# Kernel optimization log

Hardware: AMD Instinct MI355X
Metric: run time of the kernel (lower is better)

Reference implementation:

```python
import jax, jax.numpy as jnp
import numpy as np
from jax import lax

KSIZE = 3
STRIDE = 1
RATE = 2
FUSE_K = 3
SCALE = 10.0
DN = ('NCHW', 'OIHW', 'NCHW')


def _same_pad_amount(size, k, s):
    out = (size + s - 1) // s
    pad = max(0, (out - 1) * s + k - size)
    return pad // 2, pad - pad // 2


def extract_patches(x, k, s):
    # torch.nn.Unfold with 'same' padding; returns [B, L, C, k, k], L row-major
    B, C, H, W = x.shape
    pt, pb = _same_pad_amount(H, k, s)
    pl, pr = _same_pad_amount(W, k, s)
    xp = jnp.pad(x, ((0, 0), (0, 0), (pt, pb), (pl, pr)))
    Ho = (H + s - 1) // s
    Wo = (W + s - 1) // s
    rows = (jnp.arange(Ho) * s)[:, None] + jnp.arange(k)[None, :]  # [Ho,k]
    cols = (jnp.arange(Wo) * s)[:, None] + jnp.arange(k)[None, :]  # [Wo,k]
    p = xp[:, :, rows, :][:, :, :, :, cols]  # [B,C,Ho,k,Wo,k]
    return p.transpose(0, 2, 4, 1, 3, 5).reshape(B, Ho * Wo, C, k, k)


def setup_inputs() -> dict:
    key = jax.random.key(0)
    kf, kb = jax.random.split(key)
    f = jax.random.normal(kf, (2, 128, 128, 128), dtype=jnp.float32)
    b = jax.random.normal(kb, (2, 128, 128, 128), dtype=jnp.float32)
    mask = jnp.zeros((1, 1, 128, 128), dtype=jnp.float32)  # all patches available
    return {"f": f, "b": b, "mask": mask}


def reference(f, b, mask):
    B, C, Hr, Wr = f.shape
    kernel = 2 * RATE
    # raw background patches for final aggregation: [B, Lb, C, 4, 4]
    raw_w = extract_patches(b, kernel, RATE * STRIDE)
    # nearest downsample by rate (src_idx = i*rate)
    f_ds = f[:, :, ::RATE, ::RATE]
    b_ds = b[:, :, ::RATE, ::RATE]
    Hf, Wf = f_ds.shape[2], f_ds.shape[3]
    Hb, Wb = b_ds.shape[2], b_ds.shape[3]
    L = Hb * Wb
    # matching patches: [B, L, C, 3, 3]
    w = extract_patches(b_ds, KSIZE, STRIDE)
    # mask patches (shared across batch, torch uses m[0])
    m_ds = mask[:, :, ::RATE, ::RATE]
    m = extract_patches(m_ds, KSIZE, STRIDE)[0]  # [L,1,3,3]
    mm = (jnp.mean(m, axis=(1, 2, 3)) == 0.0).astype(f.dtype).reshape(1, L, 1, 1)
    # L2-normalize patch filters (escape_NaN added elementwise before sum, as in torch)
    wn = w / jnp.sqrt(jnp.sum(w * w + 1e-4, axis=(2, 3, 4), keepdims=True))

    def score_one(xi, wi):
        # xi [C,Hf,Wf], wi [L,C,3,3] -> [L,Hf,Wf]
        return lax.conv_general_dilated(xi[None], wi, (1, 1), [(1, 1), (1, 1)],
                                        dimension_numbers=DN)[0]

    y = jax.vmap(score_one)(f_ds, wn)  # [B, L, Hf, Wf]

    # diagonal fuse: identity 3x3 conv on the [L, Hf*Wf] score matrix, twice with transpose
    fw = jnp.eye(FUSE_K, dtype=f.dtype).reshape(1, 1, FUSE_K, FUSE_K)

    def fuse_conv(t):
        return lax.conv_general_dilated(t, fw, (1, 1), [(1, 1), (1, 1)],
                                        dimension_numbers=DN)

    y = y.reshape(B, 1, Hb * Wb, Hf * Wf)
    y = fuse_conv(y).reshape(B, Hb, Wb, Hf, Wf)
    y = y.transpose(0, 2, 1, 4, 3).reshape(B, 1, L, Hf * Wf)
    y = fuse_conv(y).reshape(B, Wb, Hb, Wf, Hf)
    y = y.transpose(0, 2, 1, 4, 3).reshape(B, L, Hf, Wf)

    y = y * mm
    y = jax.nn.softmax(y * SCALE, axis=1) * mm

    def deconv_one(a, wc):
        # conv_transpose2d(a, wc, stride=rate, padding=1); wc [L,C,4,4]
        wt = jnp.flip(wc, (-2, -1)).transpose(1, 0, 2, 3)  # [C,L,4,4]
        pad = kernel - 1 - 1
        return lax.conv_general_dilated(a[None], wt, (1, 1), [(pad, pad), (pad, pad)],
                                        lhs_dilation=(RATE, RATE),
                                        dimension_numbers=DN)[0]

    out = jax.vmap(deconv_one)(y, raw_w) / 4.0  # [B, C, Hr, Wr]
    return out
```

## Files before the change

kernel.cpp:

```cpp
#include <hip/hip_runtime.h>
#include <cstdint>

typedef _Float16 f16x8 __attribute__((ext_vector_type(8)));
typedef float f32x4 __attribute__((ext_vector_type(4)));

typedef __attribute__((address_space(1))) void gvoid;
typedef __attribute__((address_space(3))) void lvoid;

__device__ __forceinline__ void gload16(const void* g, void* l) {
    __builtin_amdgcn_global_load_lds((gvoid*)g, (lvoid*)l, 16, 0, 0);
}

__device__ __forceinline__ void bar() {
    asm volatile("" ::: "memory");
    __builtin_amdgcn_s_barrier();
    asm volatile("" ::: "memory");
}
#define WAITV(N) asm volatile("s_waitcnt vmcnt(" #N ")" ::: "memory")

__global__ __launch_bounds__(256) void downsample_kernel(const float* __restrict__ f,
                                                         const float* __restrict__ b,
                                                         float* __restrict__ fds,
                                                         float* __restrict__ bds) {
    int idx = blockIdx.x * 256 + threadIdx.x;
    const float* src = blockIdx.y ? b : f;
    float* dst = blockIdx.y ? bds : fds;
    int bb = idx >> 19;
    int r = idx & 524287;
    int c = r >> 12, a = (r >> 6) & 63, v = r & 63;
    dst[idx] = src[(size_t)bb * 2097152 + (size_t)c * 16384 + (2 * a) * 128 + 2 * v];
}

__global__ __launch_bounds__(256) void build_mm_kernel(const float* __restrict__ mask,
                                                       float* __restrict__ mm) {
    int l = blockIdx.x * 256 + threadIdx.x;
    if (l >= 4096) return;
    int i = l >> 6, j = l & 63;
    float s = 0.f;
    #pragma unroll
    for (int dy = 0; dy < 3; ++dy)
        #pragma unroll
        for (int dx = 0; dx < 3; ++dx) {
            int a = i + dy - 1, b = j + dx - 1;
            if ((unsigned)a < 64u && (unsigned)b < 64u)
                s += mask[(2 * a) * 128 + 2 * b];
        }
    mm[l] = (s == 0.0f) ? 1.0f : 0.0f;
}

__global__ __launch_bounds__(256) void build_fpatch_kernel(const float* __restrict__ fds,
                                                           _Float16* __restrict__ Fp) {
    int bb = blockIdx.x >> 12;
    int p = blockIdx.x & 4095;
    const float* fb = fds + (size_t)bb * 524288;
    _Float16* Fpb = Fp + (size_t)bb * 4718592;
    int u = p >> 6, v = p & 63;
    for (int k = threadIdx.x; k < 1152; k += 256) {
        int c = k / 9;
        int s = k - 9 * c;
        int dy = s / 3, dx = s - 3 * dy;
        int a = u + dy - 1, bcol = v + dx - 1;
        float val = 0.f;
        if ((unsigned)a < 64u && (unsigned)bcol < 64u)
            val = fb[c * 4096 + a * 64 + bcol];
        Fpb[(size_t)p * 1152 + k] = (_Float16)val;
    }
}

__global__ __launch_bounds__(256) void build_wn_kernel(const float* __restrict__ bds,
                                                       _Float16* __restrict__ Wn) {
    __shared__ float wsh[1152];
    __shared__ float red[4];
    int bb = blockIdx.x >> 12;
    int l = blockIdx.x & 4095;
    const float* bp = bds + (size_t)bb * 524288;
    _Float16* Wnb = Wn + (size_t)bb * 4718592;
    int i = l >> 6, j = l & 63;
    float sq = 0.f;
    for (int k = threadIdx.x; k < 1152; k += 256) {
        int c = k / 9;
        int s = k - 9 * c;
        int dy = s / 3, dx = s - 3 * dy;
        int a = i + dy - 1, bcol = j + dx - 1;
        float val = 0.f;
        if ((unsigned)a < 64u && (unsigned)bcol < 64u)
            val = bp[c * 4096 + a * 64 + bcol];
        wsh[k] = val;
        sq += val * val;
    }
    #pragma unroll
    for (int off = 32; off > 0; off >>= 1) sq += __shfl_xor(sq, off);
    if ((threadIdx.x & 63) == 0) red[threadIdx.x >> 6] = sq;
    __syncthreads();
    float total = red[0] + red[1] + red[2] + red[3] + 0.1152f;
    float rinv = 1.0f / sqrtf(total);
    for (int k = threadIdx.x; k < 1152; k += 256)
        Wnb[(size_t)l * 1152 + k] = (_Float16)(wsh[k] * rinv);
}

__global__ __launch_bounds__(256) void build_vt_kernel(const float* __restrict__ b,
                                                       _Float16* __restrict__ Vt) {
    int bb = blockIdx.x >> 11;
    int n = blockIdx.x & 2047;
    const float* bp = b + (size_t)bb * 2097152;
    _Float16* Vtb = Vt + (size_t)bb * 8388608;
    int c = n >> 4, r = n & 15, rh = r >> 2, rw = r & 3;
    const float* bc = bp + (size_t)c * 16384;
    for (int l = threadIdx.x; l < 4096; l += 256) {
        int lh = l >> 6, lw = l & 63;
        int row = 2 * lh + rh - 1, col = 2 * lw + rw - 1;
        float val = 0.f;
        if ((unsigned)row < 128u && (unsigned)col < 128u)
            val = bc[row * 128 + col];
        Vtb[(size_t)n * 4096 + l] = (_Float16)val;
    }
}

__global__ __launch_bounds__(256) void gemm1_kernel(const _Float16* __restrict__ Fp,
                                                    const _Float16* __restrict__ Wn,
                                                    _Float16* __restrict__ S0) {
    __shared__ __align__(16) _Float16 As[128 * 32];
    __shared__ __align__(16) _Float16 Bs[128 * 32];
    const int z = blockIdx.z;
    const _Float16* A = Fp + (size_t)z * 4718592;
    const _Float16* Bt = Wn + (size_t)z * 4718592;
    _Float16* C = S0 + (size_t)z * 16777216;
    const int tid = threadIdx.x;
    const int lane = tid & 63;
    const int wave = tid >> 6;
    const int quad = lane >> 4;
    const int l16 = lane & 15;
    const int bm = blockIdx.y * 128;
    const int bn = blockIdx.x * 128;
    const int waveM = (wave >> 1) * 64;
    const int waveN = (wave & 1) * 64;
    const int K = 1152;

    f32x4 acc[4][4] = {};

    const int rowS = tid >> 2;
    const int colS = (tid & 3) * 8;

    for (int k0 = 0; k0 < K; k0 += 32) {
        #pragma unroll
        for (int i = 0; i < 2; ++i) {
            const _Float16* g = A + (size_t)(bm + i * 64 + rowS) * K + k0 + colS;
            gload16(g, &As[i * 2048 + tid * 8]);
        }
        #pragma unroll
        for (int i = 0; i < 2; ++i) {
            const _Float16* g = Bt + (size_t)(bn + i * 64 + rowS) * K + k0 + colS;
            gload16(g, &Bs[i * 2048 + tid * 8]);
        }
        __syncthreads();
        f16x8 a_frag[4], b_frag[4];
        #pragma unroll
        for (int mi = 0; mi < 4; ++mi)
            a_frag[mi] = *(const f16x8*)&As[(waveM + mi * 16 + l16) * 32 + quad * 8];
        #pragma unroll
        for (int ni = 0; ni < 4; ++ni)
            b_frag[ni] = *(const f16x8*)&Bs[(waveN + ni * 16 + l16) * 32 + quad * 8];
        #pragma unroll
        for (int mi = 0; mi < 4; ++mi)
            #pragma unroll
            for (int ni = 0; ni < 4; ++ni)
                acc[mi][ni] = __builtin_amdgcn_mfma_f32_16x16x32_f16(
                    a_frag[mi], b_frag[ni], acc[mi][ni], 0, 0, 0);
        __syncthreads();
    }

    #pragma unroll
    for (int mi = 0; mi < 4; ++mi)
        #pragma unroll
        for (int ni = 0; ni < 4; ++ni)
            #pragma unroll
            for (int r = 0; r < 4; ++r) {
                int row = bm + waveM + mi * 16 + quad * 4 + r;
                int col = bn + waveN + ni * 16 + l16;
                C[(size_t)row * 4096 + col] = (_Float16)acc[mi][ni][r];
            }
}

__global__ __launch_bounds__(512, 2) void gemm2_kernel(const _Float16* __restrict__ Vt,
                                                       const _Float16* __restrict__ att0,
                                                       const _Float16* __restrict__ att1,
                                                       _Float16* __restrict__ OTh) {
    __shared__ __align__(16) _Float16 As[2][2][8192];
    __shared__ __align__(16) _Float16 Bs[2][2][8192];
    const int z = blockIdx.z;
    const _Float16* A = Vt + (size_t)z * 8388608;
    const _Float16* Bt = z ? att1 : att0;
    _Float16* C = OTh + (size_t)z * 8388608;
    const int tid = threadIdx.x;
    const int lane = tid & 63;
    const int wave = tid >> 6;
    const int quad = lane >> 4;
    const int l16 = lane & 15;
    const int wm = wave >> 2;
    const int wn = wave & 3;
    const int bm = blockIdx.y * 256;
    const int bn = blockIdx.x * 256;

    f32x4 acc[8][4] = {};
    f16x8 afr[4], bfr[4];

    const int s0 = tid, s1 = 512 + tid;
    const int sr0 = s0 >> 2, sr1 = s1 >> 2;
    const int r0 = sr0 ^ ((sr0 >> 2) & 1);
    const int r1 = sr1 ^ ((sr1 >> 2) & 1);
    const int q0 = (s0 & 3) ^ (r0 & 3);
    const int q1 = (s1 & 3) ^ (r1 & 3);
    const int offA0 = (bm + r0) * 4096 + q0 * 8;
    const int offA1 = (bm + r1) * 4096 + q1 * 8;
    const int offB0 = (bn + r0) * 4096 + q0 * 8;
    const int offB1 = (bn + r1) * 4096 + q1 * 8;

#define STAGE_A(buf, kt, kh) do {                                          \
        gload16(A + offA0 + (kt) * 64 + (kh) * 32, &As[buf][kh][tid * 8]); \
        gload16(A + offA1 + (kt) * 64 + (kh) * 32, &As[buf][kh][4096 + tid * 8]); \
    } while (0)
#define STAGE_B(buf, kt, kh) do {                                          \
        gload16(Bt + offB0 + (kt) * 64 + (kh) * 32, &Bs[buf][kh][tid * 8]); \
        gload16(Bt + offB1 + (kt) * 64 + (kh) * 32, &Bs[buf][kh][4096 + tid * 8]); \
    } while (0)

    const int c2 = (l16 >> 2) & 1;
    const int rdoff = ((l16 ^ c2) * 32) + ((quad ^ (l16 & 3)) * 8);

    auto LDA = [&](int buf, int kh, int mh) {
        #pragma unroll
        for (int mi = 0; mi < 4; ++mi)
            afr[mi] = *(const f16x8*)&As[buf][kh][(wm * 128 + (mh * 4 + mi) * 16) * 32 + rdoff];
    };
    auto LDB = [&](int buf, int kh) {
        #pragma unroll
        for (int ni = 0; ni < 4; ++ni)
            bfr[ni] = *(const f16x8*)&Bs[buf][kh][(wn * 64 + ni * 16) * 32 + rdoff];
    };
    auto MM = [&](int mh) {
        __builtin_amdgcn_s_setprio(1);
        #pragma unroll
        for (int mi = 0; mi < 4; ++mi)
            #pragma unroll
            for (int ni = 0; ni < 4; ++ni)
                acc[mh * 4 + mi][ni] = __builtin_amdgcn_mfma_f32_16x16x32_f16(
                    afr[mi], bfr[ni], acc[mh * 4 + mi][ni], 0, 0, 0);
        __builtin_amdgcn_s_setprio(0);
    };

    STAGE_A(0, 0, 0); STAGE_B(0, 0, 0);
    STAGE_A(0, 0, 1); STAGE_B(0, 0, 1);
    STAGE_A(1, 1, 0); STAGE_B(1, 1, 0);
    WAITV(4);
    bar();

    #pragma unroll 1
    for (int i = 0; i < 31; ++i) {
        const int t0 = 2 * i;
        LDA(0, 0, 0); LDB(0, 0); STAGE_A(1, t0 + 1, 1);
        bar(); MM(0); bar();
        LDA(0, 0, 1); STAGE_B(1, t0 + 1, 1);
        bar(); MM(1); bar();
        LDA(0, 1, 0); LDB(0, 1); STAGE_A(0, t0 + 2, 0);
        bar(); MM(0); bar();
        LDA(0, 1, 1); STAGE_B(0, t0 + 2, 0);
        bar(); MM(1); WAITV(4); bar();
        LDA(1, 0, 0); LDB(1, 0); STAGE_A(0, t0 + 2, 1);
        bar(); MM(0); bar();
        LDA(1, 0, 1); STAGE_B(0, t0 + 2, 1);
        bar(); MM(1); bar();
        LDA(1, 1, 0); LDB(1, 1); STAGE_A(1, t0 + 3, 0);
        bar(); MM(0); bar();
        LDA(1, 1, 1); STAGE_B(1, t0 + 3, 0);
        bar(); MM(1); WAITV(4); bar();
    }

    LDA(0, 0, 0); LDB(0, 0); STAGE_A(1, 63, 1);
    bar(); MM(0); bar();
    LDA(0, 0, 1); STAGE_B(1, 63, 1);
    bar(); MM(1); bar();
    LDA(0, 1, 0); LDB(0, 1);
    bar(); MM(0); bar();
    LDA(0, 1, 1);
    bar(); MM(1); WAITV(0); bar();
    LDA(1, 0, 0); LDB(1, 0); bar(); MM(0); bar();
    LDA(1, 0, 1);            bar(); MM(1); bar();
    LDA(1, 1, 0); LDB(1, 1); bar(); MM(0); bar();
    LDA(1, 1, 1);            bar(); MM(1); bar();

#undef STAGE_A
#undef STAGE_B

    #pragma unroll
    for (int mi = 0; mi < 8; ++mi)
        #pragma unroll
        for (int ni = 0; ni < 4; ++ni)
            #pragma unroll
            for (int r = 0; r < 4; ++r) {
                int row = bm + wm * 128 + mi * 16 + quad * 4 + r;
                int col = bn + wn * 64 + ni * 16 + l16;
                C[(size_t)row * 4096 + col] = (_Float16)acc[mi][ni][r];
            }
}

__global__ __launch_bounds__(256) void fuse_softmax_kernel(const _Float16* __restrict__ S0,
                                                           const float* __restrict__ mm,
                                                           _Float16* __restrict__ att0,
                                                           _Float16* __restrict__ att1) {
    __shared__ float red[4];
    const int tid = threadIdx.x;
    const int lane = tid & 63;
    const int wave = tid >> 6;
    int g = blockIdx.x;
    int p_global = ((g & 7) << 10) | (g >> 3);
    const int bb = p_global >> 12;
    const int p = p_global & 4095;
    const _Float16* S = S0 + (size_t)bb * 16777216;
    _Float16* att = bb ? att1 : att0;
    const int pbase = ((p & 63) << 6) | (p >> 6);

    float acc[16];
    #pragma unroll
    for (int k = 0; k < 16; ++k) acc[k] = 0.f;

    #pragma unroll
    for (int t2 = -1; t2 <= 1; ++t2) {
        int b2 = pbase + t2;
        if ((unsigned)b2 >= 4096u) continue;
        int pp = ((b2 & 63) << 6) | (b2 >> 6);
        #pragma unroll
        for (int t1 = -1; t1 <= 1; ++t1) {
            int rr = pp + t1;
            if ((unsigned)rr >= 4096u) continue;
            const _Float16* row = S + (size_t)rr * 4096;
            #pragma unroll
            for (int k = 0; k < 16; ++k) {
                int l = k * 256 + tid;
                int i = (k * 256 + wave * 64) >> 6;
                int it2 = i + t2;
                if (it2 >= 0 && it2 < 64) {
                    int c = l + t2 * 64 + t1;
                    if ((unsigned)c < 4096u)
                        acc[k] += (float)row[c];
                } else if (it2 == 64) {
                    if (lane <= 62) {
                        int c = lane + 1 + t1;
                        if ((unsigned)c < 4096u) acc[k] += (float)row[c];
                    }
                } else {
                    if (lane >= 1) {
                        int c = 4031 + lane + t1;
                        if ((unsigned)c < 4096u) acc[k] += (float)row[c];
                    }
                }
            }
        }
    }

    float mv[16];
    float lmax = -1e30f;
    #pragma unroll
    for (int k = 0; k < 16; ++k) {
        int l = k * 256 + tid;
        mv[k] = mm[l];
        float lg = acc[k] * mv[k] * 10.0f;
        acc[k] = lg;
        lmax = fmaxf(lmax, lg);
    }
    #pragma unroll
    for (int off = 32; off > 0; off >>= 1) lmax = fmaxf(lmax, __shfl_xor(lmax, off));
    if (lane == 0) red[wave] = lmax;
    __syncthreads();
    lmax = fmaxf(fmaxf(red[0], red[1]), fmaxf(red[2], red[3]));
    __syncthreads();

    float lsum = 0.f;
    #pragma unroll
    for (int k = 0; k < 16; ++k) {
        float e = __expf(acc[k] - lmax);
        acc[k] = e;
        lsum += e;
    }
    #pragma unroll
    for (int off = 32; off > 0; off >>= 1) lsum += __shfl_xor(lsum, off);
    if (lane == 0) red[wave] = lsum;
    __syncthreads();
    float inv = 1.0f / (red[0] + red[1] + red[2] + red[3]);
    #pragma unroll
    for (int k = 0; k < 16; ++k) {
        int l = k * 256 + tid;
        att[(size_t)p * 4096 + l] = (_Float16)(acc[k] * inv * mv[k]);
    }
}

__global__ __launch_bounds__(256) void assemble_kernel(const _Float16* __restrict__ OTh,
                                                       float* __restrict__ out) {
    int idx = blockIdx.x * 256 + threadIdx.x;
    int bb = idx >> 21;
    int w = idx & 2097151;
    const _Float16* OTb = OTh + (size_t)bb * 8388608;
    int x = w & 127, y = (w >> 7) & 127, c = w >> 14;
    int r0 = (y + 1) & 1, s0 = (x + 1) & 1;
    float acc = 0.f;
    #pragma unroll
    for (int a = 0; a < 2; ++a) {
        int rh = r0 + 2 * a;
        int ph = (y + 1 - rh) >> 1;
        if ((unsigned)ph < 64u) {
            #pragma unroll
            for (int bq = 0; bq < 2; ++bq) {
                int rw = s0 + 2 * bq;
                int pw = (x + 1 - rw) >> 1;
                if ((unsigned)pw < 64u)
                    acc += (float)OTb[(size_t)(c * 16 + rh * 4 + rw) * 4096 + ph * 64 + pw];
            }
        }
    }
    out[idx] = 0.25f * acc;
}

extern "C" void kernel_launch(void* const* d_in, const int* in_sizes, int n_in,
                              void* d_out, int out_size, void* d_ws, size_t ws_size,
                              hipStream_t stream) {
    const float* f = (const float*)d_in[0];
    const float* b = (const float*)d_in[1];
    const float* mask = (const float*)d_in[2];
    float* out = (float*)d_out;
    char* ws = (char*)d_ws;

    float* mm = (float*)ws;
    _Float16* Fp = (_Float16*)(ws + 16384);
    _Float16* Wn = (_Float16*)(ws + 16384 + 18874368);
    _Float16* att0 = (_Float16*)(ws + 16384);
    _Float16* S0 = (_Float16*)(ws + 37765120);
    _Float16* Vt = (_Float16*)(ws + 37765120);
    _Float16* OTh = (_Float16*)(ws + 37765120 + 33554432);
    float* fds = (float*)(ws + 104873984);
    float* bds = (float*)(ws + 104873984 + 4194304);
    _Float16* att1 = (_Float16*)(ws + 104873984);

    downsample_kernel<<<dim3(4096, 2), 256, 0, stream>>>(f, b, fds, bds);
    build_mm_kernel<<<16, 256, 0, stream>>>(mask, mm);
    build_fpatch_kernel<<<8192, 256, 0, stream>>>(fds, Fp);
    build_wn_kernel<<<8192, 256, 0, stream>>>(bds, Wn);

    gemm1_kernel<<<dim3(32, 32, 2), 256, 0, stream>>>(Fp, Wn, S0);
    fuse_softmax_kernel<<<8192, 256, 0, stream>>>(S0, mm, att0, att1);

    build_vt_kernel<<<4096, 256, 0, stream>>>(b, Vt);
    gemm2_kernel<<<dim3(16, 8, 2), 512, 0, stream>>>(Vt, att0, att1, OTh);
    assemble_kernel<<<16384, 256, 0, stream>>>(OTh, out);
}
```

Measured before the change: 438.6 us.

## Rewrite score GEMM with 256x256 tiles, double-buffered LDS and swizzled layout

```diff
diff --git a/kernel.cpp b/kernel.cpp
--- a/kernel.cpp
+++ b/kernel.cpp
@@ -116,11 +116,11 @@
     }
 }
 
-__global__ __launch_bounds__(256) void gemm1_kernel(const _Float16* __restrict__ Fp,
-                                                    const _Float16* __restrict__ Wn,
-                                                    _Float16* __restrict__ S0) {
-    __shared__ __align__(16) _Float16 As[128 * 32];
-    __shared__ __align__(16) _Float16 Bs[128 * 32];
+__global__ __launch_bounds__(512, 2) void gemm1_kernel(const _Float16* __restrict__ Fp,
+                                                       const _Float16* __restrict__ Wn,
+                                                       _Float16* __restrict__ S0) {
+    __shared__ __align__(16) _Float16 As[2][2][8192];
+    __shared__ __align__(16) _Float16 Bs[2][2][8192];
     const int z = blockIdx.z;
     const _Float16* A = Fp + (size_t)z * 4718592;
     const _Float16* Bt = Wn + (size_t)z * 4718592;
@@ -130,53 +130,109 @@
     const int wave = tid >> 6;
     const int quad = lane >> 4;
     const int l16 = lane & 15;
-    const int bm = blockIdx.y * 128;
-    const int bn = blockIdx.x * 128;
-    const int waveM = (wave >> 1) * 64;
-    const int waveN = (wave & 1) * 64;
-    const int K = 1152;
-
-    f32x4 acc[4][4] = {};
-
-    const int rowS = tid >> 2;
-    const int colS = (tid & 3) * 8;
-
-    for (int k0 = 0; k0 < K; k0 += 32) {
-        #pragma unroll
-        for (int i = 0; i < 2; ++i) {
-            const _Float16* g = A + (size_t)(bm + i * 64 + rowS) * K + k0 + colS;
-            gload16(g, &As[i * 2048 + tid * 8]);
-        }
-        #pragma unroll
-        for (int i = 0; i < 2; ++i) {
-            const _Float16* g = Bt + (size_t)(bn + i * 64 + rowS) * K + k0 + colS;
-            gload16(g, &Bs[i * 2048 + tid * 8]);
-        }
-        __syncthreads();
-        f16x8 a_frag[4], b_frag[4];
+    const int wm = wave >> 2;
+    const int wn = wave & 3;
+    const int bm = blockIdx.y * 256;
+    const int bn = blockIdx.x * 256;
+
+    f32x4 acc[8][4] = {};
+    f16x8 afr[4], bfr[4];
+
+    const int s0 = tid, s1 = 512 + tid;
+    const int sr0 = s0 >> 2, sr1 = s1 >> 2;
+    const int r0 = sr0 ^ ((sr0 >> 2) & 1);
+    const int r1 = sr1 ^ ((sr1 >> 2) & 1);
+    const int q0 = (s0 & 3) ^ (r0 & 3);
+    const int q1 = (s1 & 3) ^ (r1 & 3);
+    const int offA0 = (bm + r0) * 1152 + q0 * 8;
+    const int offA1 = (bm + r1) * 1152 + q1 * 8;
+    const int offB0 = (bn + r0) * 1152 + q0 * 8;
+    const int offB1 = (bn + r1) * 1152 + q1 * 8;
+
+#define STAGE_A(buf, kt, kh) do {                                          \
+        gload16(A + offA0 + (kt) * 64 + (kh) * 32, &As[buf][kh][tid * 8]); \
+        gload16(A + offA1 + (kt) * 64 + (kh) * 32, &As[buf][kh][4096 + tid * 8]); \
+    } while (0)
+#define STAGE_B(buf, kt, kh) do {                                          \
+        gload16(Bt + offB0 + (kt) * 64 + (kh) * 32, &Bs[buf][kh][tid * 8]); \
+        gload16(Bt + offB1 + (kt) * 64 + (kh) * 32, &Bs[buf][kh][4096 + tid * 8]); \
+    } while (0)
+
+    const int c2 = (l16 >> 2) & 1;
+    const int rdoff = ((l16 ^ c2) * 32) + ((quad ^ (l16 & 3)) * 8);
+
+    auto LDA = [&](int buf, int kh, int mh) {
         #pragma unroll
         for (int mi = 0; mi < 4; ++mi)
-            a_frag[mi] = *(const f16x8*)&As[(waveM + mi * 16 + l16) * 32 + quad * 8];
+            afr[mi] = *(const f16x8*)&As[buf][kh][(wm * 128 + (mh * 4 + mi) * 16) * 32 + rdoff];
+    };
+    auto LDB = [&](int buf, int kh) {
         #pragma unroll
         for (int ni = 0; ni < 4; ++ni)
-            b_frag[ni] = *(const f16x8*)&Bs[(waveN + ni * 16 + l16) * 32 + quad * 8];
+            bfr[ni] = *(const f16x8*)&Bs[buf][kh][(wn * 64 + ni * 16) * 32 + rdoff];
+    };
+    auto MM = [&](int mh) {
+        __builtin_amdgcn_s_setprio(1);
         #pragma unroll
         for (int mi = 0; mi < 4; ++mi)
             #pragma unroll
             for (int ni = 0; ni < 4; ++ni)
-                acc[mi][ni] = __builtin_amdgcn_mfma_f32_16x16x32_f16(
-                    a_frag[mi], b_frag[ni], acc[mi][ni], 0, 0, 0);
-        __syncthreads();
-    }
-
-    #pragma unroll
-    for (int mi = 0; mi < 4; ++mi)
+                acc[mh * 4 + mi][ni] = __builtin_amdgcn_mfma_f32_16x16x32_f16(
+                    afr[mi], bfr[ni], acc[mh * 4 + mi][ni], 0, 0, 0);
+        __builtin_amdgcn_s_setprio(0);
+    };
+
+    STAGE_A(0, 0, 0); STAGE_B(0, 0, 0);
+    STAGE_A(0, 0, 1); STAGE_B(0, 0, 1);
+    STAGE_A(1, 1, 0); STAGE_B(1, 1, 0);
+    WAITV(4);
+    bar();
+
+    #pragma unroll 1
+    for (int i = 0; i < 8; ++i) {
+        const int t0 = 2 * i;
+        LDA(0, 0, 0); LDB(0, 0); STAGE_A(1, t0 + 1, 1);
+        bar(); MM(0); bar();
+        LDA(0, 0, 1); STAGE_B(1, t0 + 1, 1);
+        bar(); MM(1); bar();
+        LDA(0, 1, 0); LDB(0, 1); STAGE_A(0, t0 + 2, 0);
+        bar(); MM(0); bar();
+        LDA(0, 1, 1); STAGE_B(0, t0 + 2, 0);
+        bar(); MM(1); WAITV(4); bar();
+        LDA(1, 0, 0); LDB(1, 0); STAGE_A(0, t0 + 2, 1);
+        bar(); MM(0); bar();
+        LDA(1, 0, 1); STAGE_B(0, t0 + 2, 1);
+        bar(); MM(1); bar();
+        LDA(1, 1, 0); LDB(1, 1); STAGE_A(1, t0 + 3, 0);
+        bar(); MM(0); bar();
+        LDA(1, 1, 1); STAGE_B(1, t0 + 3, 0);
+        bar(); MM(1); WAITV(4); bar();
+    }
+
+    LDA(0, 0, 0); LDB(0, 0); STAGE_A(1, 17, 1);
+    bar(); MM(0); bar();
+    LDA(0, 0, 1); STAGE_B(1, 17, 1);
+    bar(); MM(1); bar();
+    LDA(0, 1, 0); LDB(0, 1);
+    bar(); MM(0); bar();
+    LDA(0, 1, 1);
+    bar(); MM(1); WAITV(0); bar();
+    LDA(1, 0, 0); LDB(1, 0); bar(); MM(0); bar();
+    LDA(1, 0, 1);            bar(); MM(1); bar();
+    LDA(1, 1, 0); LDB(1, 1); bar(); MM(0); bar();
+    LDA(1, 1, 1);            bar(); MM(1); bar();
+
+#undef STAGE_A
+#undef STAGE_B
+
+    #pragma unroll
+    for (int mi = 0; mi < 8; ++mi)
         #pragma unroll
         for (int ni = 0; ni < 4; ++ni)
             #pragma unroll
             for (int r = 0; r < 4; ++r) {
-                int row = bm + waveM + mi * 16 + quad * 4 + r;
-                int col = bn + waveN + ni * 16 + l16;
+                int row = bm + wm * 128 + mi * 16 + quad * 4 + r;
+                int col = bn + wn * 64 + ni * 16 + l16;
                 C[(size_t)row * 4096 + col] = (_Float16)acc[mi][ni][r];
             }
 }
@@ -444,7 +500,7 @@
     build_fpatch_kernel<<<8192, 256, 0, stream>>>(fds, Fp);
     build_wn_kernel<<<8192, 256, 0, stream>>>(bds, Wn);
 
-    gemm1_kernel<<<dim3(32, 32, 2), 256, 0, stream>>>(Fp, Wn, S0);
+    gemm1_kernel<<<dim3(16, 16, 2), 512, 0, stream>>>(Fp, Wn, S0);
     fuse_softmax_kernel<<<8192, 256, 0, stream>>>(S0, mm, att0, att1);
 
     build_vt_kernel<<<4096, 256, 0, stream>>>(b, Vt);
```

New measurement: 434.2 us. About the same (-1.0%).

## Share pipelined 256x256 GEMM core across both GEMMs with register double-buffered fragments

Applied to the files above, without the earlier changes.

```diff
diff --git a/kernel.cpp b/kernel.cpp
--- a/kernel.cpp
+++ b/kernel.cpp
@@ -116,81 +116,12 @@
     }
 }
 
-__global__ __launch_bounds__(256) void gemm1_kernel(const _Float16* __restrict__ Fp,
-                                                    const _Float16* __restrict__ Wn,
-                                                    _Float16* __restrict__ S0) {
-    __shared__ __align__(16) _Float16 As[128 * 32];
-    __shared__ __align__(16) _Float16 Bs[128 * 32];
-    const int z = blockIdx.z;
-    const _Float16* A = Fp + (size_t)z * 4718592;
-    const _Float16* Bt = Wn + (size_t)z * 4718592;
-    _Float16* C = S0 + (size_t)z * 16777216;
-    const int tid = threadIdx.x;
-    const int lane = tid & 63;
-    const int wave = tid >> 6;
-    const int quad = lane >> 4;
-    const int l16 = lane & 15;
-    const int bm = blockIdx.y * 128;
-    const int bn = blockIdx.x * 128;
-    const int waveM = (wave >> 1) * 64;
-    const int waveN = (wave & 1) * 64;
-    const int K = 1152;
-
-    f32x4 acc[4][4] = {};
-
-    const int rowS = tid >> 2;
-    const int colS = (tid & 3) * 8;
-
-    for (int k0 = 0; k0 < K; k0 += 32) {
-        #pragma unroll
-        for (int i = 0; i < 2; ++i) {
-            const _Float16* g = A + (size_t)(bm + i * 64 + rowS) * K + k0 + colS;
-            gload16(g, &As[i * 2048 + tid * 8]);
-        }
-        #pragma unroll
-        for (int i = 0; i < 2; ++i) {
-            const _Float16* g = Bt + (size_t)(bn + i * 64 + rowS) * K + k0 + colS;
-            gload16(g, &Bs[i * 2048 + tid * 8]);
-        }
-        __syncthreads();
-        f16x8 a_frag[4], b_frag[4];
-        #pragma unroll
-        for (int mi = 0; mi < 4; ++mi)
-            a_frag[mi] = *(const f16x8*)&As[(waveM + mi * 16 + l16) * 32 + quad * 8];
-        #pragma unroll
-        for (int ni = 0; ni < 4; ++ni)
-            b_frag[ni] = *(const f16x8*)&Bs[(waveN + ni * 16 + l16) * 32 + quad * 8];
-        #pragma unroll
-        for (int mi = 0; mi < 4; ++mi)
-            #pragma unroll
-            for (int ni = 0; ni < 4; ++ni)
-                acc[mi][ni] = __builtin_amdgcn_mfma_f32_16x16x32_f16(
-                    a_frag[mi], b_frag[ni], acc[mi][ni], 0, 0, 0);
-        __syncthreads();
-    }
-
-    #pragma unroll
-    for (int mi = 0; mi < 4; ++mi)
-        #pragma unroll
-        for (int ni = 0; ni < 4; ++ni)
-            #pragma unroll
-            for (int r = 0; r < 4; ++r) {
-                int row = bm + waveM + mi * 16 + quad * 4 + r;
-                int col = bn + waveN + ni * 16 + l16;
-                C[(size_t)row * 4096 + col] = (_Float16)acc[mi][ni][r];
-            }
-}
-
-__global__ __launch_bounds__(512, 2) void gemm2_kernel(const _Float16* __restrict__ Vt,
-                                                       const _Float16* __restrict__ att0,
-                                                       const _Float16* __restrict__ att1,
-                                                       _Float16* __restrict__ OTh) {
-    __shared__ __align__(16) _Float16 As[2][2][8192];
-    __shared__ __align__(16) _Float16 Bs[2][2][8192];
-    const int z = blockIdx.z;
-    const _Float16* A = Vt + (size_t)z * 8388608;
-    const _Float16* Bt = z ? att1 : att0;
-    _Float16* C = OTh + (size_t)z * 8388608;
+template <int KSTR, int NTILES>
+__device__ __forceinline__ void gemm_core(const _Float16* __restrict__ A,
+                                          const _Float16* __restrict__ Bt,
+                                          _Float16* __restrict__ C,
+                                          _Float16* __restrict__ AsB,
+                                          _Float16* __restrict__ BsB) {
     const int tid = threadIdx.x;
     const int lane = tid & 63;
     const int wave = tid >> 6;
@@ -202,7 +133,7 @@
     const int bn = blockIdx.x * 256;
 
     f32x4 acc[8][4] = {};
-    f16x8 afr[4], bfr[4];
+    f16x8 afr[2][4], bfr[2][4];
 
     const int s0 = tid, s1 = 512 + tid;
     const int sr0 = s0 >> 2, sr1 = s1 >> 2;
@@ -210,86 +141,91 @@
     const int r1 = sr1 ^ ((sr1 >> 2) & 1);
     const int q0 = (s0 & 3) ^ (r0 & 3);
     const int q1 = (s1 & 3) ^ (r1 & 3);
-    const int offA0 = (bm + r0) * 4096 + q0 * 8;
-    const int offA1 = (bm + r1) * 4096 + q1 * 8;
-    const int offB0 = (bn + r0) * 4096 + q0 * 8;
-    const int offB1 = (bn + r1) * 4096 + q1 * 8;
-
-#define STAGE_A(buf, kt, kh) do {                                          \
-        gload16(A + offA0 + (kt) * 64 + (kh) * 32, &As[buf][kh][tid * 8]); \
-        gload16(A + offA1 + (kt) * 64 + (kh) * 32, &As[buf][kh][4096 + tid * 8]); \
+    const int offA0 = (bm + r0) * KSTR + q0 * 8;
+    const int offA1 = (bm + r1) * KSTR + q1 * 8;
+    const int offB0 = (bn + r0) * KSTR + q0 * 8;
+    const int offB1 = (bn + r1) * KSTR + q1 * 8;
+
+#define STAGE_A(buf, kt, kh) do {                                                          \
+        gload16(A + offA0 + (kt) * 64 + (kh) * 32, AsB + ((buf) * 2 + (kh)) * 8192 + tid * 8); \
+        gload16(A + offA1 + (kt) * 64 + (kh) * 32, AsB + ((buf) * 2 + (kh)) * 8192 + 4096 + tid * 8); \
     } while (0)
-#define STAGE_B(buf, kt, kh) do {                                          \
-        gload16(Bt + offB0 + (kt) * 64 + (kh) * 32, &Bs[buf][kh][tid * 8]); \
-        gload16(Bt + offB1 + (kt) * 64 + (kh) * 32, &Bs[buf][kh][4096 + tid * 8]); \
+#define STAGE_B(buf, kt, kh) do {                                                          \
+        gload16(Bt + offB0 + (kt) * 64 + (kh) * 32, BsB + ((buf) * 2 + (kh)) * 8192 + tid * 8); \
+        gload16(Bt + offB1 + (kt) * 64 + (kh) * 32, BsB + ((buf) * 2 + (kh)) * 8192 + 4096 + tid * 8); \
     } while (0)
 
     const int c2 = (l16 >> 2) & 1;
     const int rdoff = ((l16 ^ c2) * 32) + ((quad ^ (l16 & 3)) * 8);
 
-    auto LDA = [&](int buf, int kh, int mh) {
-        #pragma unroll
-        for (int mi = 0; mi < 4; ++mi)
-            afr[mi] = *(const f16x8*)&As[buf][kh][(wm * 128 + (mh * 4 + mi) * 16) * 32 + rdoff];
-    };
-    auto LDB = [&](int buf, int kh) {
-        #pragma unroll
-        for (int ni = 0; ni < 4; ++ni)
-            bfr[ni] = *(const f16x8*)&Bs[buf][kh][(wn * 64 + ni * 16) * 32 + rdoff];
-    };
-    auto MM = [&](int mh) {
-        __builtin_amdgcn_s_setprio(1);
-        #pragma unroll
-        for (int mi = 0; mi < 4; ++mi)
-            #pragma unroll
-            for (int ni = 0; ni < 4; ++ni)
-                acc[mh * 4 + mi][ni] = __builtin_amdgcn_mfma_f32_16x16x32_f16(
-                    afr[mi], bfr[ni], acc[mh * 4 + mi][ni], 0, 0, 0);
-        __builtin_amdgcn_s_setprio(0);
-    };
+#define LDA(par, buf, kh, mh) do {                                                         \
+        _Pragma("unroll")                                                                  \
+        for (int mi = 0; mi < 4; ++mi)                                                     \
+            afr[par][mi] = *(const f16x8*)&AsB[((buf) * 2 + (kh)) * 8192 +                 \
+                (wm * 128 + ((mh) * 4 + mi) * 16) * 32 + rdoff];                           \
+    } while (0)
+#define LDB(par, buf, kh) do {                                                             \
+        _Pragma("unroll")                                                                  \
+        for (int ni = 0; ni < 4; ++ni)                                                     \
+            bfr[par][ni] = *(const f16x8*)&BsB[((buf) * 2 + (kh)) * 8192 +                 \
+                (wn * 64 + ni * 16) * 32 + rdoff];                                         \
+    } while (0)
+#define MM(apar, bpar, mh) do {                                                            \
+        __builtin_amdgcn_s_setprio(1);                                                     \
+        _Pragma("unroll")                                                                  \
+        for (int mi = 0; mi < 4; ++mi)                                                     \
+            _Pragma("unroll")                                                              \
+            for (int ni = 0; ni < 4; ++ni)                                                 \
+                acc[(mh) * 4 + mi][ni] = __builtin_amdgcn_mfma_f32_16x16x32_f16(           \
+                    afr[apar][mi], bfr[bpar][ni], acc[(mh) * 4 + mi][ni], 0, 0, 0);        \
+        __builtin_amdgcn_s_setprio(0);                                                     \
+    } while (0)
 
     STAGE_A(0, 0, 0); STAGE_B(0, 0, 0);
     STAGE_A(0, 0, 1); STAGE_B(0, 0, 1);
     STAGE_A(1, 1, 0); STAGE_B(1, 1, 0);
     WAITV(4);
     bar();
+    LDA(0, 0, 0, 0); LDB(0, 0, 0);
 
     #pragma unroll 1
-    for (int i = 0; i < 31; ++i) {
+    for (int i = 0; i < NTILES / 2 - 1; ++i) {
         const int t0 = 2 * i;
-        LDA(0, 0, 0); LDB(0, 0); STAGE_A(1, t0 + 1, 1);
-        bar(); MM(0); bar();
-        LDA(0, 0, 1); STAGE_B(1, t0 + 1, 1);
-        bar(); MM(1); bar();
-        LDA(0, 1, 0); LDB(0, 1); STAGE_A(0, t0 + 2, 0);
-        bar(); MM(0); bar();
-        LDA(0, 1, 1); STAGE_B(0, t0 + 2, 0);
-        bar(); MM(1); WAITV(4); bar();
-        LDA(1, 0, 0); LDB(1, 0); STAGE_A(0, t0 + 2, 1);
-        bar(); MM(0); bar();
-        LDA(1, 0, 1); STAGE_B(0, t0 + 2, 1);
-        bar(); MM(1); bar();
-        LDA(1, 1, 0); LDB(1, 1); STAGE_A(1, t0 + 3, 0);
-        bar(); MM(0); bar();
-        LDA(1, 1, 1); STAGE_B(1, t0 + 3, 0);
-        bar(); MM(1); WAITV(4); bar();
-    }
-
-    LDA(0, 0, 0); LDB(0, 0); STAGE_A(1, 63, 1);
-    bar(); MM(0); bar();
-    LDA(0, 0, 1); STAGE_B(1, 63, 1);
-    bar(); MM(1); bar();
-    LDA(0, 1, 0); LDB(0, 1);
-    bar(); MM(0); bar();
-    LDA(0, 1, 1);
-    bar(); MM(1); WAITV(0); bar();
-    LDA(1, 0, 0); LDB(1, 0); bar(); MM(0); bar();
-    LDA(1, 0, 1);            bar(); MM(1); bar();
-    LDA(1, 1, 0); LDB(1, 1); bar(); MM(0); bar();
-    LDA(1, 1, 1);            bar(); MM(1); bar();
+        STAGE_A(1, t0 + 1, 1); bar();
+        LDA(1, 0, 0, 1); MM(0, 0, 0); bar();
+        STAGE_B(1, t0 + 1, 1); bar();
+        LDA(0, 0, 1, 0); LDB(1, 0, 1); MM(1, 0, 1); bar();
+        STAGE_A(0, t0 + 2, 0); bar();
+        LDA(1, 0, 1, 1); MM(0, 1, 0); bar();
+        STAGE_B(0, t0 + 2, 0); WAITV(4); bar();
+        LDA(0, 1, 0, 0); LDB(0, 1, 0); MM(1, 1, 1); bar();
+        STAGE_A(0, t0 + 2, 1); bar();
+        LDA(1, 1, 0, 1); MM(0, 0, 0); bar();
+        STAGE_B(0, t0 + 2, 1); bar();
+        LDA(0, 1, 1, 0); LDB(1, 1, 1); MM(1, 0, 1); bar();
+        STAGE_A(1, t0 + 3, 0); bar();
+        LDA(1, 1, 1, 1); MM(0, 1, 0); bar();
+        STAGE_B(1, t0 + 3, 0); WAITV(4); bar();
+        LDA(0, 0, 0, 0); LDB(0, 0, 0); MM(1, 1, 1); bar();
+    }
+
+    STAGE_A(1, NTILES - 1, 1); bar();
+    LDA(1, 0, 0, 1); MM(0, 0, 0); bar();
+    STAGE_B(1, NTILES - 1, 1); bar();
+    LDA(0, 0, 1, 0); LDB(1, 0, 1); MM(1, 0, 1); bar();
+    LDA(1, 0, 1, 1); MM(0, 1, 0); bar();
+    WAITV(0); bar();
+    LDA(0, 1, 0, 0); LDB(0, 1, 0); MM(1, 1, 1); bar();
+    LDA(1, 1, 0, 1); MM(0, 0, 0); bar();
+    LDA(0, 1, 1, 0); LDB(1, 1, 1); MM(1, 0, 1); bar();
+    LDA(1, 1, 1, 1); MM(0, 1, 0); bar();
+    MM(1, 1, 1);
 
 #undef STAGE_A
 #undef STAGE_B
+#undef LDA
+#undef LDB
+#undef MM
 
     #pragma unroll
     for (int mi = 0; mi < 8; ++mi)
@@ -301,6 +237,27 @@
                 int col = bn + wn * 64 + ni * 16 + l16;
                 C[(size_t)row * 4096 + col] = (_Float16)acc[mi][ni][r];
             }
+}
+
+__global__ __launch_bounds__(512, 2) void gemm1_kernel(const _Float16* __restrict__ Fp,
+                                                       const _Float16* __restrict__ Wn,
+                                                       _Float16* __restrict__ S0) {
+    __shared__ __align__(16) _Float16 As[2][2][8192];
+    __shared__ __align__(16) _Float16 Bs[2][2][8192];
+    const int z = blockIdx.z;
+    gemm_core<1152, 18>(Fp + (size_t)z * 4718592, Wn + (size_t)z * 4718592,
+                        S0 + (size_t)z * 16777216, &As[0][0][0], &Bs[0][0][0]);
+}
+
+__global__ __launch_bounds__(512, 2) void gemm2_kernel(const _Float16* __restrict__ Vt,
+                                                       const _Float16* __restrict__ att0,
+                                                       const _Float16* __restrict__ att1,
+                                                       _Float16* __restrict__ OTh) {
+    __shared__ __align__(16) _Float16 As[2][2][8192];
+    __shared__ __align__(16) _Float16 Bs[2][2][8192];
+    const int z = blockIdx.z;
+    gemm_core<4096, 64>(Vt + (size_t)z * 8388608, z ? att1 : att0,
+                        OTh + (size_t)z * 8388608, &As[0][0][0], &Bs[0][0][0]);
 }
 
 __global__ __launch_bounds__(256) void fuse_softmax_kernel(const _Float16* __restrict__ S0,
@@ -444,7 +401,7 @@
     build_fpatch_kernel<<<8192, 256, 0, stream>>>(fds, Fp);
     build_wn_kernel<<<8192, 256, 0, stream>>>(bds, Wn);
 
-    gemm1_kernel<<<dim3(32, 32, 2), 256, 0, stream>>>(Fp, Wn, S0);
+    gemm1_kernel<<<dim3(16, 16, 2), 512, 0, stream>>>(Fp, Wn, S0);
     fuse_softmax_kernel<<<8192, 256, 0, stream>>>(S0, mm, att0, att1);
 
     build_vt_kernel<<<4096, 256, 0, stream>>>(b, Vt);
```

Result: no change. 431.1 us (-1.7%).
